# Performance work log

Hardware: AMD Instinct MI355X
Metric: run time of the kernel (lower is better)

The kernel has to match this reference:

```python
import jax, jax.numpy as jnp
import numpy as np

T, D, H = 1024, 256, 256


def mish(x):
    return x * jnp.tanh(jax.nn.softplus(x))


def layer_norm(x, w, b, eps=1e-5):
    mu = x.mean(-1, keepdims=True)
    var = ((x - mu) ** 2).mean(-1, keepdims=True)
    return (x - mu) / jnp.sqrt(var + eps) * w + b


def setup_inputs() -> dict:
    key = jax.random.key(0)
    ks = jax.random.split(key, 12)
    def glorot(k, sh, fan_in):
        return (jax.random.normal(k, sh, jnp.float32) / np.sqrt(fan_in)).astype(jnp.float32)
    return {
        "x": jax.random.normal(ks[0], (T, D), jnp.float32),
        "s0": jnp.zeros((1, H, H), jnp.float32),
        "z0": jnp.zeros((1, H), jnp.float32),
        "start": jax.random.randint(ks[1], (T + 1,), 0, 2, jnp.int32),
        "done": jax.random.randint(ks[2], (T + 1,), 0, 2, jnp.int32),
        "Wk": glorot(ks[3], (H, D), D),
        "Wq": glorot(ks[4], (H, D), D),
        "Wv": glorot(ks[5], (H, D), D),
        "Wskip": glorot(ks[6], (H, D), D),
        "bskip": jnp.zeros((H,), jnp.float32),
        "W1": glorot(ks[7], (H, H), H),
        "b1": jnp.zeros((H,), jnp.float32),
        "W2": glorot(ks[8], (H, H), H),
        "b2": jnp.zeros((H,), jnp.float32),
        "W3": glorot(ks[9], (H, H), H),
        "b3": jnp.zeros((H,), jnp.float32),
        "ln_w": jnp.ones((H,), jnp.float32),
        "ln_b": jnp.zeros((H,), jnp.float32),
    }


def reference(x, s0, z0, start, done, Wk, Wq, Wv, Wskip, bskip, W1, b1, W2, b2, W3, b3, ln_w, ln_b):
    # feature maps (equinox Linear: y = W @ x, weight is (out,in))
    k = jax.nn.elu(x @ Wk.T)          # [T,H]
    q = jax.nn.elu(x @ Wq.T)          # [T,H]
    v = x @ Wv.T                      # [T,H]
    st = start.astype(x.dtype)[:, None]   # [T+1,1] reset-continuation flags
    dn = done.astype(x.dtype)[:, None]    # [T+1,1]
    # prepend carried state to the sequence, as in the original
    kv = jnp.concatenate([s0, jnp.einsum('ti,tj->tij', k, v)], axis=0)  # [T+1,H,H]
    kk = jnp.concatenate([z0, k], axis=0)                               # [T+1,H]
    def combine(a, b):
        s_a, z_a, _, _ = a
        kv_b, k_b, st_b, dn_b = b
        s = s_a * st_b[..., None] + kv_b * dn_b[..., None]
        z = z_a * st_b + k_b * dn_b
        return (s, z, st_b, dn_b)
    s, z, _, _ = jax.lax.associative_scan(combine, (kv, kk, st, dn))
    # drop the initial-state slot so time indices align with queries
    s_t, z_t = s[1:], z[1:]                          # [T,H,H], [T,H]
    numer = jnp.einsum('ti,tij->tj', q, s_t)         # [T,H]
    denom = jnp.einsum('ti,tj->t', z_t, q).clip(1e-5)  # faithful to source einsum
    out = numer / denom[:, None]
    h = mish(out @ W1.T + b1)
    h = mish(h @ W2.T + b2)
    h = h @ W3.T + b3
    return layer_norm(h + (x @ Wskip.T + bskip), ln_w, ln_b)
```

## Files before the change

kernel.cpp:

```cpp
#include <hip/hip_runtime.h>
#include <math.h>


typedef unsigned long long u64;
typedef unsigned short u16;
typedef __attribute__((ext_vector_type(8))) unsigned short us8;
typedef __attribute__((ext_vector_type(4))) unsigned short us4;
typedef __attribute__((ext_vector_type(8))) short s8;
typedef __attribute__((ext_vector_type(4))) float f4;

__device__ __forceinline__ float eluf(float v) { return v > 0.f ? v : expm1f(v); }
__device__ __forceinline__ float mishf(float v) {
  float sp = fmaxf(v, 0.f) + log1pf(expf(-fabsf(v)));
  return v * tanhf(sp);
}
__device__ __forceinline__ u16 f2bf(float f) {
  unsigned u = __float_as_uint(f);
  unsigned r = u + 0x7FFFu + ((u >> 16) & 1u);
  return (u16)(r >> 16);
}
__device__ __forceinline__ float bf2f(u16 h) { return __uint_as_float((unsigned)h << 16); }

__device__ __forceinline__ f4 mfma16(const u16* a, const u16* b, f4 c) {
  s8 av = *(const s8*)(const void*)a;
  s8 bv = *(const s8*)(const void*)b;
  return __builtin_amdgcn_mfma_f32_16x16x32_bf16(av, bv, c, 0, 0, 0);
}

__device__ __forceinline__ u64 expand32(u64 x) {
  x &= 0xFFFFFFFFull;
  x = (x | (x << 16)) & 0x0000FFFF0000FFFFull;
  x = (x | (x << 8))  & 0x00FF00FF00FF00FFull;
  x = (x | (x << 4))  & 0x0F0F0F0F0F0F0F0Full;
  x = (x | (x << 2))  & 0x3333333333333333ull;
  x = (x | (x << 1))  & 0x5555555555555555ull;
  return x | (x << 1);
}

__device__ __forceinline__ us8 cvt8v(float4 a, float4 b) {
  us8 v;
  v[0] = f2bf(a.x); v[1] = f2bf(a.y); v[2] = f2bf(a.z); v[3] = f2bf(a.w);
  v[4] = f2bf(b.x); v[5] = f2bf(b.y); v[6] = f2bf(b.z); v[7] = f2bf(b.w);
  return v;
}

__global__ __launch_bounds__(256) void qkvs_mfma(const float* __restrict__ x,
    const float* __restrict__ Wk, const float* __restrict__ Wq,
    const float* __restrict__ Wv, const float* __restrict__ Wsk,
    const float* __restrict__ bskip,
    const float* __restrict__ W1, const float* __restrict__ W2, const float* __restrict__ W3,
    u16* __restrict__ Kb, u16* __restrict__ Qb, u16* __restrict__ Vb,
    float* __restrict__ SKP, float* __restrict__ Kpart, u16* __restrict__ Wb) {
  __shared__ u16 Xs[64 * 40], Ws[64 * 40];
  const int tid = threadIdx.x, wave = tid >> 6, l = tid & 63;
  const int l15 = l & 15, quad = l >> 4;
  const int rt = blockIdx.x & 15, my = blockIdx.x >> 4;
  const int mat = my >> 2, nt = my & 3;
  const int n0 = nt * 64, mbase = rt * 64;
  const float* Wsrc = (mat == 0) ? Wk : (mat == 1) ? Wq : (mat == 2) ? Wv : Wsk;
  if (tid < 192) {
    int cidx = blockIdx.x * 768 + tid * 4;
    const float* Wm = (cidx < 65536) ? W1 : (cidx < 131072) ? W2 : W3;
    float4 v = *(const float4*)(Wm + (cidx & 65535));
    us4 o; o.x = f2bf(v.x); o.y = f2bf(v.y); o.z = f2bf(v.z); o.w = f2bf(v.w);
    *(us4*)&Wb[cidx] = o;
  }
  f4 acc[4];
#pragma unroll
  for (int s = 0; s < 4; s++) acc[s] = (f4){0.f, 0.f, 0.f, 0.f};
  const int srow = tid >> 2, sko = (tid & 3) * 8;
  const float* xp = &x[(mbase + srow) * 256 + sko];
  const float* wp = &Wsrc[(n0 + srow) * 256 + sko];
  float4 xa = *(const float4*)xp, xb = *(const float4*)(xp + 4);
  float4 wa = *(const float4*)wp, wc = *(const float4*)(wp + 4);
#pragma unroll 1
  for (int kt = 0; kt < 8; kt++) {
    *(us8*)&Xs[srow * 40 + sko] = cvt8v(xa, xb);
    *(us8*)&Ws[srow * 40 + sko] = cvt8v(wa, wc);
    if (kt < 7) {
      xa = *(const float4*)(xp + (kt + 1) * 32);
      xb = *(const float4*)(xp + (kt + 1) * 32 + 4);
      wa = *(const float4*)(wp + (kt + 1) * 32);
      wc = *(const float4*)(wp + (kt + 1) * 32 + 4);
    }
    __syncthreads();
    const u16* ap = &Xs[(wave * 16 + l15) * 40 + quad * 8];
#pragma unroll
    for (int s = 0; s < 4; s++)
      acc[s] = mfma16(ap, &Ws[(s * 16 + l15) * 40 + quad * 8], acc[s]);
    __syncthreads();
  }
  const int mw = mbase + wave * 16 + quad * 4;
  if (mat == 0) {
    float tmp[4][4];
#pragma unroll
    for (int s = 0; s < 4; s++)
#pragma unroll
      for (int r = 0; r < 4; r++) {
        float v = eluf(acc[s][r]);
        tmp[s][r] = v;
        Kb[(mw + r) * 256 + n0 + s * 16 + l15] = f2bf(v);
      }
#pragma unroll
    for (int r = 0; r < 4; r++) {
      float t = tmp[0][r] + tmp[1][r] + tmp[2][r] + tmp[3][r];
#pragma unroll
      for (int off = 1; off <= 8; off <<= 1) t += __shfl_xor(t, off);
      if (l15 == 0) Kpart[nt * 1024 + mw + r] = t;
    }
  } else if (mat == 1) {
#pragma unroll
    for (int s = 0; s < 4; s++)
#pragma unroll
      for (int r = 0; r < 4; r++)
        Qb[(mw + r) * 256 + n0 + s * 16 + l15] = f2bf(eluf(acc[s][r]));
  } else if (mat == 2) {
#pragma unroll
    for (int s = 0; s < 4; s++)
#pragma unroll
      for (int r = 0; r < 4; r++)
        Vb[(mw + r) * 256 + n0 + s * 16 + l15] = f2bf(acc[s][r]);
  } else {
#pragma unroll
    for (int s = 0; s < 4; s++) {
      int n = n0 + s * 16 + l15;
      float bv = bskip[n];
#pragma unroll
      for (int r = 0; r < 4; r++)
        SKP[(mw + r) * 256 + n] = acc[s][r] + bv;
    }
  }
}

__global__ __launch_bounds__(512) void attn_mlp(
    const u16* __restrict__ Kb, const u16* __restrict__ Qb, const u16* __restrict__ Vb,
    const float* __restrict__ Kpart, const float* __restrict__ SKP,
    const int* __restrict__ start, const int* __restrict__ done,
    const u16* __restrict__ Wb,
    const float* __restrict__ b1, const float* __restrict__ b2, const float* __restrict__ b3,
    const float* __restrict__ lnw, const float* __restrict__ lnb,
    float* __restrict__ outp) {
  __shared__ float Ks[1024];
  __shared__ unsigned char sBs[1028], dBs[1028];
  __shared__ u64 GS[37];
  __shared__ u64 CH[2][21];
  __shared__ u64 Mw[32];
  __shared__ u16 As[16 * 264];
  __shared__ float Op[8][256];
  __shared__ float dp[8];
  __shared__ float Hbuf[2 * 260];
  const int tid = threadIdx.x, wave = tid >> 6, l = tid & 63;
  const int l15 = l & 15, quad = l >> 4;
  const int m0 = blockIdx.x * 2;
  for (int i = tid; i < 1025; i += 512) {
    sBs[i] = (unsigned char)(start[i] != 0);
    dBs[i] = (unsigned char)(done[i] != 0);
  }
  {
    int j = tid * 2;
    Ks[j] = Kpart[j] + Kpart[1024 + j] + Kpart[2048 + j] + Kpart[3072 + j];
    Ks[j + 1] = Kpart[j + 1] + Kpart[1024 + j + 1] + Kpart[2048 + j + 1] + Kpart[3072 + j + 1];
  }
  if (wave < 2 && l == 0) CH[wave][20] = 1ull;
  __syncthreads();
  if (wave >= 2) {
    for (int job = wave - 2; job < 37; job += 6) {
      int lv, w;
      if (job < 17)      { lv = 0; w = job; }
      else if (job < 25) { lv = 1; w = job - 17; }
      else if (job < 29) { lv = 2; w = job - 25; }
      else if (job < 31) { lv = 3; w = job - 29; }
      else               { lv = job - 27; w = 0; }
      int n = 1024 >> lv;
      int j = w * 64 + l;
      int ok = 0;
      if (j < n)
        ok = (j & 1) ? dBs[((j + 1) << lv) - 1] : sBs[((j + 2) << lv) - 1];
      u64 word = __ballot(ok != 0);
      if (l == 0) GS[(lv == 0) ? w : (lv == 1) ? 17 + w : (lv == 2) ? 25 + w
                     : (lv == 3) ? 29 + w : 27 + lv] = word;
    }
  }
  __syncthreads();
  const int CHOFF[11] = {0, 0, 8, 12, 14, 15, 16, 17, 18, 19, 20};
  const int GOFF2[10] = {0, 17, 25, 29, 31, 32, 33, 34, 35, 36};
#pragma unroll 1
  for (int lv = 9; lv >= 1; lv--) {
    if (wave < 2) {
      int nw = (1024 >> lv) >= 64 ? ((1024 >> lv) >> 6) : 1;
      if (l < nw) {
        int rr = m0 + wave + 1;
        for (int q = 0; q < lv; q++) rr = (rr & 1) ? (rr >> 1) : (rr >> 1) - 1;
        u64 word;
        if (rr <= 0) word = (l == 0 && rr == 0) ? 1ull : 0ull;
        else {
          u64 pw = CH[wave][CHOFF[lv + 1] + (l >> 1)];
          u64 e = expand32((l & 1) ? (pw >> 32) : pw) & GS[GOFF2[lv] + l];
          if (rr & 1) word = e;
          else {
            int gi = ((rr + 1) << lv) - 1;
            word = sBs[gi] ? e : 0ull;
            if ((rr >> 6) == l) word |= (u64)dBs[gi] << (rr & 63);
          }
        }
        CH[wave][CHOFF[lv] + l] = word;
      }
    }
    __syncthreads();
  }
  if (wave < 2) {
    const int t = m0 + wave + 1;
    u64 uw = 0;
    if (l <= 16) {
      u64 e = 0;
      if (l < 16) {
        u64 pw = CH[wave][(l >> 1)];
        e = expand32((l & 1) ? (pw >> 32) : pw) & GS[l];
      }
      if (t & 1) uw = e;
      else {
        uw = sBs[t] ? e : 0ull;
        if ((t >> 6) == l) uw |= (u64)dBs[t] << (t & 63);
      }
    }
    u64 nxt = __shfl(uw, (l + 1) & 63);
    u64 mw0 = (uw >> 1) | (nxt << 63);
    if (l < 16) Mw[wave * 16 + l] = mw0;
  }
  __syncthreads();
  const int r = wave & 1, h = wave >> 1;
  const int tp = m0 + r;
  float q[4], O[4] = {0.f, 0.f, 0.f, 0.f};
  {
    us4 qv = *(const us4*)&Qb[tp * 256 + l * 4];
    q[0] = bf2f(qv.x); q[1] = bf2f(qv.y); q[2] = bf2f(qv.z); q[3] = bf2f(qv.w);
  }
  float qs = q[0] + q[1] + q[2] + q[3];
#pragma unroll
  for (int off = 1; off <= 32; off <<= 1) qs += __shfl_xor(qs, off);
  float d = 0.f;
  for (int w = h * 4; w < h * 4 + 4; w++) {
    u64 bits = Mw[r * 16 + w];
    while (bits) {
      int b0 = __builtin_ctzll(bits); bits &= bits - 1;
      int j0 = w * 64 + b0;
      if (bits) {
        int b1x = __builtin_ctzll(bits); bits &= bits - 1;
        int j1 = w * 64 + b1x;
        us4 k0 = *(const us4*)&Kb[j0 * 256 + l * 4];
        us4 v0 = *(const us4*)&Vb[j0 * 256 + l * 4];
        us4 k1 = *(const us4*)&Kb[j1 * 256 + l * 4];
        us4 v1 = *(const us4*)&Vb[j1 * 256 + l * 4];
        float s0 = q[0] * bf2f(k0.x) + q[1] * bf2f(k0.y) + q[2] * bf2f(k0.z) + q[3] * bf2f(k0.w);
        float s1 = q[0] * bf2f(k1.x) + q[1] * bf2f(k1.y) + q[2] * bf2f(k1.z) + q[3] * bf2f(k1.w);
#pragma unroll
        for (int off = 1; off <= 32; off <<= 1) {
          s0 += __shfl_xor(s0, off);
          s1 += __shfl_xor(s1, off);
        }
        d += Ks[j0] + Ks[j1];
        O[0] += s0 * bf2f(v0.x) + s1 * bf2f(v1.x);
        O[1] += s0 * bf2f(v0.y) + s1 * bf2f(v1.y);
        O[2] += s0 * bf2f(v0.z) + s1 * bf2f(v1.z);
        O[3] += s0 * bf2f(v0.w) + s1 * bf2f(v1.w);
      } else {
        us4 k0 = *(const us4*)&Kb[j0 * 256 + l * 4];
        us4 v0 = *(const us4*)&Vb[j0 * 256 + l * 4];
        float s0 = q[0] * bf2f(k0.x) + q[1] * bf2f(k0.y) + q[2] * bf2f(k0.z) + q[3] * bf2f(k0.w);
#pragma unroll
        for (int off = 1; off <= 32; off <<= 1) s0 += __shfl_xor(s0, off);
        d += Ks[j0];
        O[0] += s0 * bf2f(v0.x); O[1] += s0 * bf2f(v0.y);
        O[2] += s0 * bf2f(v0.z); O[3] += s0 * bf2f(v0.w);
      }
    }
  }
#pragma unroll
  for (int i = 0; i < 4; i++) Op[wave][l * 4 + i] = O[i];
  if (l == 0) dp[wave] = d;
  __syncthreads();
  if (h == 0) {
    float dd = dp[r] + dp[r + 2] + dp[r + 4] + dp[r + 6];
    float inv = 1.f / fmaxf(qs * dd, 1e-5f);
    us4 o;
    o.x = f2bf((O[0] + Op[r + 2][l * 4 + 0] + Op[r + 4][l * 4 + 0] + Op[r + 6][l * 4 + 0]) * inv);
    o.y = f2bf((O[1] + Op[r + 2][l * 4 + 1] + Op[r + 4][l * 4 + 1] + Op[r + 6][l * 4 + 1]) * inv);
    o.z = f2bf((O[2] + Op[r + 2][l * 4 + 2] + Op[r + 4][l * 4 + 2] + Op[r + 6][l * 4 + 2]) * inv);
    o.w = f2bf((O[3] + Op[r + 2][l * 4 + 3] + Op[r + 4][l * 4 + 3] + Op[r + 6][l * 4 + 3]) * inv);
    *(us4*)&As[r * 264 + l * 4] = o;
  }
  __syncthreads();
#pragma unroll 1
  for (int layer = 0; layer < 3; layer++) {
    const u16* Wl = Wb + layer * 65536;
    const float* bias = (layer == 0) ? b1 : (layer == 1) ? b2 : b3;
    f4 acc[2];
#pragma unroll
    for (int c = 0; c < 2; c++) {
      const int nt = wave * 2 + c;
      acc[c] = (f4){0.f, 0.f, 0.f, 0.f};
#pragma unroll
      for (int kt = 0; kt < 8; kt++) {
        us8 bf = *(const us8*)&Wl[(nt * 16 + l15) * 256 + kt * 32 + quad * 8];
        acc[c] = mfma16(&As[l15 * 264 + kt * 32 + quad * 8], (const u16*)&bf, acc[c]);
      }
    }
    __syncthreads();
    if (quad == 0) {
#pragma unroll
      for (int c = 0; c < 2; c++) {
        const int n = (wave * 2 + c) * 16 + l15;
        float bv = bias[n];
        if (layer < 2) {
#pragma unroll
          for (int rr = 0; rr < 2; rr++)
            As[rr * 264 + n] = f2bf(mishf(acc[c][rr] + bv));
        } else {
#pragma unroll
          for (int rr = 0; rr < 2; rr++)
            Hbuf[rr * 260 + n] = acc[c][rr] + bv + SKP[(m0 + rr) * 256 + n];
        }
      }
    }
    __syncthreads();
  }
  if (wave < 2) {
    float hv[4];
#pragma unroll
    for (int i = 0; i < 4; i++) hv[i] = Hbuf[wave * 260 + l * 4 + i];
    float s1 = hv[0] + hv[1] + hv[2] + hv[3];
    float s2 = hv[0] * hv[0] + hv[1] * hv[1] + hv[2] * hv[2] + hv[3] * hv[3];
#pragma unroll
    for (int off = 1; off <= 32; off <<= 1) {
      s1 += __shfl_xor(s1, off);
      s2 += __shfl_xor(s2, off);
    }
    float mu = s1 * (1.f / 256.f);
    float var = s2 * (1.f / 256.f) - mu * mu;
    float rs = rsqrtf(fmaxf(var, 0.f) + 1e-5f);
    float4 wv = *(const float4*)&lnw[l * 4];
    float4 bv = *(const float4*)&lnb[l * 4];
    float4 o;
    o.x = (hv[0] - mu) * rs * wv.x + bv.x;
    o.y = (hv[1] - mu) * rs * wv.y + bv.y;
    o.z = (hv[2] - mu) * rs * wv.z + bv.z;
    o.w = (hv[3] - mu) * rs * wv.w + bv.w;
    *(float4*)&outp[(m0 + wave) * 256 + l * 4] = o;
  }
}

extern "C" void kernel_launch(void* const* d_in, const int* in_sizes, int n_in,
                              void* d_out, int out_size, void* d_ws, size_t ws_size,
                              hipStream_t stream) {
  (void)in_sizes; (void)n_in; (void)out_size; (void)ws_size;
  const float* x   = (const float*)d_in[0];
  const int* start = (const int*)d_in[3];
  const int* done  = (const int*)d_in[4];
  const float* Wk  = (const float*)d_in[5];
  const float* Wq  = (const float*)d_in[6];
  const float* Wv  = (const float*)d_in[7];
  const float* Wsk = (const float*)d_in[8];
  const float* bsk = (const float*)d_in[9];
  const float* W1  = (const float*)d_in[10];
  const float* b1  = (const float*)d_in[11];
  const float* W2  = (const float*)d_in[12];
  const float* b2  = (const float*)d_in[13];
  const float* W3  = (const float*)d_in[14];
  const float* b3  = (const float*)d_in[15];
  const float* lnw = (const float*)d_in[16];
  const float* lnb = (const float*)d_in[17];
  float* out = (float*)d_out;

  char* w = (char*)d_ws;
  u16* Kb      = (u16*)w;
  u16* Qb      = (u16*)(w + 524288);
  u16* Vb      = (u16*)(w + 1048576);
  float* SKP   = (float*)(w + 1572864);
  float* Kpart = (float*)(w + 2621440);
  u16* Wb      = (u16*)(w + 2637824);

  qkvs_mfma<<<256, 256, 0, stream>>>(x, Wk, Wq, Wv, Wsk, bsk, W1, W2, W3,
                                     Kb, Qb, Vb, SKP, Kpart, Wb);
  attn_mlp<<<512, 512, 0, stream>>>(Kb, Qb, Vb, Kpart, SKP, start, done, Wb,
                                    b1, b2, b3, lnw, lnb, out);
}
```

Baseline: 136.7 us.

## Process four timesteps per block and compute scan chain in registers via shuffles

Each attention/MLP block now handles four query rows instead of two, halving the grid to 256 blocks. The per-level chain construction moves from shared memory with a block barrier per level to a per-wave register loop using shuffles. The shared-memory staging of start/done flags and summed Kpart is dropped in favour of direct global reads. This removes nine block-wide barriers and the staging loads, and amortizes the MLP weight reads over more rows. In exchange, each wave walks twice as many mask words, which serializes more of the attention work per wave, and the scattered global reads of Kpart and the flags add latency.

After: 129.5 us. 5.3% less time.

```diff
diff --git a/kernel.cpp b/kernel.cpp
--- a/kernel.cpp
+++ b/kernel.cpp
@@ -140,87 +140,69 @@
     const float* __restrict__ b1, const float* __restrict__ b2, const float* __restrict__ b3,
     const float* __restrict__ lnw, const float* __restrict__ lnb,
     float* __restrict__ outp) {
-  __shared__ float Ks[1024];
-  __shared__ unsigned char sBs[1028], dBs[1028];
   __shared__ u64 GS[37];
-  __shared__ u64 CH[2][21];
-  __shared__ u64 Mw[32];
+  __shared__ u64 Mw[64];
   __shared__ u16 As[16 * 264];
   __shared__ float Op[8][256];
   __shared__ float dp[8];
-  __shared__ float Hbuf[2 * 260];
+  __shared__ float Hbuf[4 * 260];
   const int tid = threadIdx.x, wave = tid >> 6, l = tid & 63;
   const int l15 = l & 15, quad = l >> 4;
-  const int m0 = blockIdx.x * 2;
-  for (int i = tid; i < 1025; i += 512) {
-    sBs[i] = (unsigned char)(start[i] != 0);
-    dBs[i] = (unsigned char)(done[i] != 0);
-  }
-  {
-    int j = tid * 2;
-    Ks[j] = Kpart[j] + Kpart[1024 + j] + Kpart[2048 + j] + Kpart[3072 + j];
-    Ks[j + 1] = Kpart[j + 1] + Kpart[1024 + j + 1] + Kpart[2048 + j + 1] + Kpart[3072 + j + 1];
-  }
-  if (wave < 2 && l == 0) CH[wave][20] = 1ull;
+  const int m0 = blockIdx.x * 4;
+  for (int job = wave; job < 37; job += 8) {
+    int lv, w;
+    if (job < 17)      { lv = 0; w = job; }
+    else if (job < 25) { lv = 1; w = job - 17; }
+    else if (job < 29) { lv = 2; w = job - 25; }
+    else if (job < 31) { lv = 3; w = job - 29; }
+    else               { lv = job - 27; w = 0; }
+    int n = 1024 >> lv;
+    int j = w * 64 + l;
+    int ok = 0;
+    if (j < n)
+      ok = (j & 1) ? (done[((j + 1) << lv) - 1] != 0) : (start[((j + 2) << lv) - 1] != 0);
+    u64 word = __ballot(ok != 0);
+    if (l == 0) GS[(lv == 0) ? w : (lv == 1) ? 17 + w : (lv == 2) ? 25 + w
+                   : (lv == 3) ? 29 + w : 27 + lv] = word;
+  }
   __syncthreads();
-  if (wave >= 2) {
-    for (int job = wave - 2; job < 37; job += 6) {
-      int lv, w;
-      if (job < 17)      { lv = 0; w = job; }
-      else if (job < 25) { lv = 1; w = job - 17; }
-      else if (job < 29) { lv = 2; w = job - 25; }
-      else if (job < 31) { lv = 3; w = job - 29; }
-      else               { lv = job - 27; w = 0; }
-      int n = 1024 >> lv;
-      int j = w * 64 + l;
-      int ok = 0;
-      if (j < n)
-        ok = (j & 1) ? dBs[((j + 1) << lv) - 1] : sBs[((j + 2) << lv) - 1];
-      u64 word = __ballot(ok != 0);
-      if (l == 0) GS[(lv == 0) ? w : (lv == 1) ? 17 + w : (lv == 2) ? 25 + w
-                     : (lv == 3) ? 29 + w : 27 + lv] = word;
-    }
-  }
-  __syncthreads();
-  const int CHOFF[11] = {0, 0, 8, 12, 14, 15, 16, 17, 18, 19, 20};
   const int GOFF2[10] = {0, 17, 25, 29, 31, 32, 33, 34, 35, 36};
+  if (wave < 4) {
+    const int t = m0 + wave + 1;
+    int rr10 = t;
+#pragma unroll
+    for (int q = 0; q < 10; q++) rr10 = (rr10 & 1) ? (rr10 >> 1) : (rr10 >> 1) - 1;
+    u64 cur = (l == 0 && rr10 == 0) ? 1ull : 0ull;
 #pragma unroll 1
-  for (int lv = 9; lv >= 1; lv--) {
-    if (wave < 2) {
-      int nw = (1024 >> lv) >= 64 ? ((1024 >> lv) >> 6) : 1;
-      if (l < nw) {
-        int rr = m0 + wave + 1;
-        for (int q = 0; q < lv; q++) rr = (rr & 1) ? (rr >> 1) : (rr >> 1) - 1;
-        u64 word;
-        if (rr <= 0) word = (l == 0 && rr == 0) ? 1ull : 0ull;
+    for (int lv = 9; lv >= 1; lv--) {
+      int rr = t;
+      for (int q = 0; q < lv; q++) rr = (rr & 1) ? (rr >> 1) : (rr >> 1) - 1;
+      const int nw = (lv >= 4) ? 1 : (8 >> (lv - 1));
+      u64 pw = __shfl(cur, l >> 1);
+      u64 word;
+      if (rr <= 0) word = (l == 0 && rr == 0) ? 1ull : 0ull;
+      else {
+        u64 e = 0;
+        if (l < nw) e = expand32((l & 1) ? (pw >> 32) : pw) & GS[GOFF2[lv] + l];
+        if (rr & 1) word = e;
         else {
-          u64 pw = CH[wave][CHOFF[lv + 1] + (l >> 1)];
-          u64 e = expand32((l & 1) ? (pw >> 32) : pw) & GS[GOFF2[lv] + l];
-          if (rr & 1) word = e;
-          else {
-            int gi = ((rr + 1) << lv) - 1;
-            word = sBs[gi] ? e : 0ull;
-            if ((rr >> 6) == l) word |= (u64)dBs[gi] << (rr & 63);
-          }
+          int gi = ((rr + 1) << lv) - 1;
+          word = (start[gi] != 0) ? e : 0ull;
+          if ((rr >> 6) == l) word |= (u64)(done[gi] != 0) << (rr & 63);
         }
-        CH[wave][CHOFF[lv] + l] = word;
-      }
-    }
-    __syncthreads();
-  }
-  if (wave < 2) {
-    const int t = m0 + wave + 1;
+        if (l >= nw) word = 0ull;
+      }
+      cur = word;
+    }
+    u64 pw = __shfl(cur, (l >> 1) & 7);
     u64 uw = 0;
     if (l <= 16) {
       u64 e = 0;
-      if (l < 16) {
-        u64 pw = CH[wave][(l >> 1)];
-        e = expand32((l & 1) ? (pw >> 32) : pw) & GS[l];
-      }
+      if (l < 16) e = expand32((l & 1) ? (pw >> 32) : pw) & GS[l];
       if (t & 1) uw = e;
       else {
-        uw = sBs[t] ? e : 0ull;
-        if ((t >> 6) == l) uw |= (u64)dBs[t] << (t & 63);
+        uw = (start[t] != 0) ? e : 0ull;
+        if ((t >> 6) == l) uw |= (u64)(done[t] != 0) << (t & 63);
       }
     }
     u64 nxt = __shfl(uw, (l + 1) & 63);
@@ -228,7 +210,7 @@
     if (l < 16) Mw[wave * 16 + l] = mw0;
   }
   __syncthreads();
-  const int r = wave & 1, h = wave >> 1;
+  const int r = wave & 3, h = wave >> 2;
   const int tp = m0 + r;
   float q[4], O[4] = {0.f, 0.f, 0.f, 0.f};
   {
@@ -239,7 +221,7 @@
 #pragma unroll
   for (int off = 1; off <= 32; off <<= 1) qs += __shfl_xor(qs, off);
   float d = 0.f;
-  for (int w = h * 4; w < h * 4 + 4; w++) {
+  for (int w = h * 8; w < h * 8 + 8; w++) {
     u64 bits = Mw[r * 16 + w];
     while (bits) {
       int b0 = __builtin_ctzll(bits); bits &= bits - 1;
@@ -258,7 +240,8 @@
           s0 += __shfl_xor(s0, off);
           s1 += __shfl_xor(s1, off);
         }
-        d += Ks[j0] + Ks[j1];
+        d += (Kpart[j0] + Kpart[1024 + j0] + Kpart[2048 + j0] + Kpart[3072 + j0]) +
+             (Kpart[j1] + Kpart[1024 + j1] + Kpart[2048 + j1] + Kpart[3072 + j1]);
         O[0] += s0 * bf2f(v0.x) + s1 * bf2f(v1.x);
         O[1] += s0 * bf2f(v0.y) + s1 * bf2f(v1.y);
         O[2] += s0 * bf2f(v0.z) + s1 * bf2f(v1.z);
@@ -269,7 +252,7 @@
         float s0 = q[0] * bf2f(k0.x) + q[1] * bf2f(k0.y) + q[2] * bf2f(k0.z) + q[3] * bf2f(k0.w);
 #pragma unroll
         for (int off = 1; off <= 32; off <<= 1) s0 += __shfl_xor(s0, off);
-        d += Ks[j0];
+        d += Kpart[j0] + Kpart[1024 + j0] + Kpart[2048 + j0] + Kpart[3072 + j0];
         O[0] += s0 * bf2f(v0.x); O[1] += s0 * bf2f(v0.y);
         O[2] += s0 * bf2f(v0.z); O[3] += s0 * bf2f(v0.w);
       }
@@ -280,13 +263,13 @@
   if (l == 0) dp[wave] = d;
   __syncthreads();
   if (h == 0) {
-    float dd = dp[r] + dp[r + 2] + dp[r + 4] + dp[r + 6];
+    float dd = dp[r] + dp[r + 4];
     float inv = 1.f / fmaxf(qs * dd, 1e-5f);
     us4 o;
-    o.x = f2bf((O[0] + Op[r + 2][l * 4 + 0] + Op[r + 4][l * 4 + 0] + Op[r + 6][l * 4 + 0]) * inv);
-    o.y = f2bf((O[1] + Op[r + 2][l * 4 + 1] + Op[r + 4][l * 4 + 1] + Op[r + 6][l * 4 + 1]) * inv);
-    o.z = f2bf((O[2] + Op[r + 2][l * 4 + 2] + Op[r + 4][l * 4 + 2] + Op[r + 6][l * 4 + 2]) * inv);
-    o.w = f2bf((O[3] + Op[r + 2][l * 4 + 3] + Op[r + 4][l * 4 + 3] + Op[r + 6][l * 4 + 3]) * inv);
+    o.x = f2bf((O[0] + Op[r + 4][l * 4 + 0]) * inv);
+    o.y = f2bf((O[1] + Op[r + 4][l * 4 + 1]) * inv);
+    o.z = f2bf((O[2] + Op[r + 4][l * 4 + 2]) * inv);
+    o.w = f2bf((O[3] + Op[r + 4][l * 4 + 3]) * inv);
     *(us4*)&As[r * 264 + l * 4] = o;
   }
   __syncthreads();
@@ -313,18 +296,18 @@
         float bv = bias[n];
         if (layer < 2) {
 #pragma unroll
-          for (int rr = 0; rr < 2; rr++)
+          for (int rr = 0; rr < 4; rr++)
             As[rr * 264 + n] = f2bf(mishf(acc[c][rr] + bv));
         } else {
 #pragma unroll
-          for (int rr = 0; rr < 2; rr++)
+          for (int rr = 0; rr < 4; rr++)
             Hbuf[rr * 260 + n] = acc[c][rr] + bv + SKP[(m0 + rr) * 256 + n];
         }
       }
     }
     __syncthreads();
   }
-  if (wave < 2) {
+  if (wave < 4) {
     float hv[4];
 #pragma unroll
     for (int i = 0; i < 4; i++) hv[i] = Hbuf[wave * 260 + l * 4 + i];
@@ -381,6 +364,6 @@
 
   qkvs_mfma<<<256, 256, 0, stream>>>(x, Wk, Wq, Wv, Wsk, bsk, W1, W2, W3,
                                      Kb, Qb, Vb, SKP, Kpart, Wb);
-  attn_mlp<<<512, 512, 0, stream>>>(Kb, Qb, Vb, Kpart, SKP, start, done, Wb,
+  attn_mlp<<<256, 512, 0, stream>>>(Kb, Qb, Vb, Kpart, SKP, start, done, Wb,
                                     b1, b2, b3, lnw, lnb, out);
 }
```
